# Kernel tuning notes

Hardware: AMD Instinct MI355X
Metric: run time of the kernel (lower is better)

Reference implementation:

```python
import jax, jax.numpy as jnp
import numpy as np
from jax import lax

B, D, H, E, TOPK = 4096, 512, 1024, 16, 4


def setup_inputs() -> dict:
    key = jax.random.key(0)
    ks = jax.random.split(key, 7)
    s = 0.02
    return {
        "x": jax.random.normal(ks[0], (B, D), jnp.float32),
        "gate_x": jax.random.normal(ks[1], (B, D), jnp.float32),
        "w_gate": jax.random.normal(ks[2], (D, E), jnp.float32) * s,
        "w1": jax.random.normal(ks[3], (E, D, H), jnp.float32) * s,
        "b1": jax.random.normal(ks[4], (E, H), jnp.float32) * s,
        "w2": jax.random.normal(ks[5], (E, H, D), jnp.float32) * s,
        "b2": jax.random.normal(ks[6], (E, D), jnp.float32) * s,
        "k": TOPK,
    }


def _cv_squared(v):
    # torch .var() is unbiased (ddof=1)
    eps = 1e-10
    return jnp.var(v, ddof=1) / (jnp.mean(v) ** 2 + eps)


def reference(x, gate_x, w_gate, w1, b1, w2, b2, k):
    # --- noisy_top_k_gating with train=False (clean logits path) ---
    logits = gate_x @ w_gate                      # [B, E]
    top_logits, top_idx = lax.top_k(logits, min(k + 1, E))
    topk_logits = top_logits[:, :k]               # [B, k]
    topk_idx = top_idx[:, :k]                     # [B, k]
    topk_gates = jax.nn.softmax(topk_logits, axis=1)
    batch_ar = jnp.arange(logits.shape[0])[:, None]
    gates = jnp.zeros_like(logits).at[batch_ar, topk_idx].set(topk_gates)  # [B, E]

    load = (gates > 0).sum(axis=0).astype(jnp.float32)   # [E]
    importance = gates.sum(axis=0)                        # [E]
    loss = _cv_squared(importance) + _cv_squared(load)

    # --- dispatch / per-expert MLP / weighted combine ---
    # Mathematically identical to SparseDispatcher: output[b] = sum_e gates[b,e]*MLP_e(x[b]).
    # Expressed as a vectorized per-expert GEMM; zero gates null out non-routed experts.
    h = jax.nn.relu(jnp.einsum('bd,edh->ebh', x, w1) + b1[:, None, :])  # [E, B, H]
    expert_out = jnp.einsum('ebh,eho->ebo', h, w2) + b2[:, None, :]      # [E, B, D]
    y = jnp.einsum('be,ebo->bo', gates, expert_out)                      # [B, D]
    return y, loss
```

## Files before the change

### kernel.cpp

```cpp
#include <hip/hip_runtime.h>
#include <cstdint>
#include <cstddef>

#define B_TOK 4096
#define DIM   512
#define HID   1024
#define NEXP  16
#define NSLOT 4

typedef __bf16 bf16x8 __attribute__((ext_vector_type(8)));
typedef float  f32x4  __attribute__((ext_vector_type(4)));
typedef unsigned short ushort8 __attribute__((ext_vector_type(8)));
typedef unsigned short ushort4v __attribute__((ext_vector_type(4)));

static __device__ __forceinline__ unsigned short f2bf(float f) {
    union { float f; unsigned u; } v; v.f = f;
    unsigned r = v.u + 0x7FFFu + ((v.u >> 16) & 1u);
    return (unsigned short)(r >> 16);
}
static __device__ __forceinline__ float bf2f(unsigned short u) {
    union { unsigned u; float f; } v; v.u = (unsigned)u << 16; return v.f;
}

static __device__ __forceinline__ void gl_lds16(const unsigned short* g, unsigned short* l) {
    __builtin_amdgcn_global_load_lds(
        (const __attribute__((address_space(1))) unsigned int*)(const void*)g,
        (__attribute__((address_space(3))) unsigned int*)(void*)l, 16, 0, 0);
}

static __device__ __forceinline__ bf16x8 fragRD(const unsigned short* s, int row, int ks) {
    int byte = row * 128 + ((ks * 2) ^ ((row & 7) << 4));
    return *(const bf16x8*)((const char*)s + byte);
}

#define LOGITS_OFF 0x0000000u
#define LTOK_OFF   0x0100000u
#define LGATE_OFF  0x0140000u
#define CTRL_OFF   0x0180000u
#define PMAP_OFF   0x01A0000u
#define XBF_OFF    0x0200000u
#define W1T_OFF    0x0600000u
#define W2T_OFF    0x1600000u
#define H_OFF      0x2600000u
#define YS_OFF     W1T_OFF

__global__ __launch_bounds__(256) void k_init(
        int* cnt, float* imp,
        const float* __restrict__ x, unsigned short* __restrict__ xbf,
        const float* __restrict__ w1, unsigned short* __restrict__ w1t,
        const float* __restrict__ gx, const float* __restrict__ wg,
        float* __restrict__ logits) {
    __shared__ unsigned short T[64][74];
    const int bid = blockIdx.x;
    const int t = threadIdx.x;
    if (bid < 1024) {
        int row = bid * 4 + (t >> 6);
        int l = t & 63;
        int e = l & 15;
        int c = l >> 4;
        const float* xr = gx + (size_t)row * DIM + c * 128;
        const float* wc = wg + (size_t)(c * 128) * NEXP + e;
        float s = 0.0f;
        #pragma unroll 8
        for (int d = 0; d < 128; d += 4) {
            float4 v = *(const float4*)(xr + d);
            s += v.x * wc[(d + 0) * NEXP] + v.y * wc[(d + 1) * NEXP]
               + v.z * wc[(d + 2) * NEXP] + v.w * wc[(d + 3) * NEXP];
        }
        s += __shfl_xor(s, 16);
        s += __shfl_xor(s, 32);
        if (l < NEXP) logits[row * NEXP + l] = s;
        return;
    }
    if (bid < 2048) {
        int i = (bid - 1024) * 256 + t;
        const float4* s = (const float4*)(x + (size_t)i * 8);
        float4 a = s[0], b = s[1];
        ushort8 v = { f2bf(a.x), f2bf(a.y), f2bf(a.z), f2bf(a.w),
                      f2bf(b.x), f2bf(b.y), f2bf(b.z), f2bf(b.w) };
        *(ushort8*)(xbf + (size_t)i * 8) = v;
        if (bid == 1024 && t < NEXP) { cnt[t] = 0; imp[t] = 0.0f; }
        return;
    }
    const int idx = bid - 2048;
    const int ktiles = DIM >> 6;
    const int e   = idx >> 7;
    const int rem = idx & 127;
    const int k0 = (rem % ktiles) * 64;
    const int n0 = (rem / ktiles) * 64;
    const int kr = t >> 4, n4 = (t & 15) * 4;
    #pragma unroll
    for (int it = 0; it < 4; it++) {
        int k = kr + it * 16;
        float4 v = *(const float4*)(w1 + ((size_t)e * DIM + k0 + k) * HID + n0 + n4);
        T[n4 + 0][k] = f2bf(v.x);
        T[n4 + 1][k] = f2bf(v.y);
        T[n4 + 2][k] = f2bf(v.z);
        T[n4 + 3][k] = f2bf(v.w);
    }
    __syncthreads();
    const int nn = t >> 3, k8 = (t & 7) * 8;
    #pragma unroll
    for (int rep = 0; rep < 2; rep++) {
        int n = nn + rep * 32;
        ushort8 o;
        #pragma unroll
        for (int i = 0; i < 8; i++) o[i] = T[n][k8 + i];
        *(ushort8*)(w1t + ((size_t)e * HID + n0 + n) * DIM + k0 + k8) = o;
    }
}

__global__ __launch_bounds__(64) void k_route(const float* __restrict__ logits,
                        int* __restrict__ cnt, float* __restrict__ imp,
                        int* __restrict__ ltok, float* __restrict__ lgate,
                        int* __restrict__ posmap) {
    __shared__ int   lcnt[NEXP];
    __shared__ float limp[NEXP];
    __shared__ int   lbase[NEXP];
    const int t = threadIdx.x;
    if (t < NEXP) { lcnt[t] = 0; limp[t] = 0.0f; }
    __syncthreads();

    const int b = blockIdx.x * 64 + t;
    const float4* lp = (const float4*)(logits + (size_t)b * NEXP);
    float4 q0 = lp[0], q1 = lp[1], q2 = lp[2], q3 = lp[3];
    float lg[NEXP] = { q0.x, q0.y, q0.z, q0.w, q1.x, q1.y, q1.z, q1.w,
                       q2.x, q2.y, q2.z, q2.w, q3.x, q3.y, q3.z, q3.w };

    int idx[NSLOT]; float val[NSLOT];
    unsigned used = 0;
    #pragma unroll
    for (int j = 0; j < NSLOT; j++) {
        float bv = -1e30f; int bi = 0;
        #pragma unroll
        for (int i = 0; i < NEXP; i++) {
            bool ok = !((used >> i) & 1u);
            if (ok && lg[i] > bv) { bv = lg[i]; bi = i; }
        }
        idx[j] = bi; val[j] = bv; used |= (1u << bi);
    }
    float m = val[0];
    float ex[NSLOT]; float sum = 0.0f;
    #pragma unroll
    for (int j = 0; j < NSLOT; j++) { ex[j] = __expf(val[j] - m); sum += ex[j]; }
    float inv = 1.0f / sum;

    int   lpos[NSLOT];
    float gv[NSLOT];
    #pragma unroll
    for (int j = 0; j < NSLOT; j++) {
        gv[j] = ex[j] * inv;
        lpos[j] = atomicAdd(&lcnt[idx[j]], 1);
        atomicAdd(&limp[idx[j]], gv[j]);
    }
    __syncthreads();
    if (t < NEXP) {
        lbase[t] = atomicAdd(&cnt[t], lcnt[t]);
        atomicAdd(&imp[t], limp[t]);
    }
    __syncthreads();
    #pragma unroll
    for (int j = 0; j < NSLOT; j++) {
        int e = idx[j];
        int p = lbase[e] + lpos[j];
        ltok[e * B_TOK + p]  = b;
        lgate[e * B_TOK + p] = gv[j];
        posmap[b * NSLOT + j] = (e << 12) | p;
    }
}

__global__ void k_prep(int* __restrict__ ctrl, float* __restrict__ out_loss) {
    const int* cnt = ctrl;
    const float* imp = (const float*)(ctrl + 16);
    int* bases = ctrl + 32;
    int* np    = ctrl + 48;
    int* pairs = ctrl + 64;
    int l = threadIdx.x;
    if (l >= 16) return;
    int base = 0, poff = 0;
    #pragma unroll
    for (int j = 0; j < 16; j++) {
        int cj = cnt[j];
        base += (j < l) ? cj : 0;
        poff += (j < l) ? ((cj + 127) >> 7) : 0;
    }
    bases[l] = base;
    int c = cnt[l];
    int ntile = (c + 127) >> 7;
    for (int i = 0; i < ntile; i++) pairs[poff + i] = (l << 16) | i;
    if (l == 15) *np = poff + ntile;

    float cf = (float)c, im = imp[l];
    float sc = cf, si = im;
    #pragma unroll
    for (int m = 8; m >= 1; m >>= 1) { sc += __shfl_xor(sc, m, 16); si += __shfl_xor(si, m, 16); }
    float ml = sc / 16.0f, mi = si / 16.0f;
    float dc = cf - ml, di = im - mi;
    float vc = dc * dc, vi = di * di;
    #pragma unroll
    for (int m = 8; m >= 1; m >>= 1) { vc += __shfl_xor(vc, m, 16); vi += __shfl_xor(vi, m, 16); }
    vc /= 15.0f; vi /= 15.0f;
    if (l == 0) *out_loss = vi / (mi * mi + 1e-10f) + vc / (ml * ml + 1e-10f);
}

__global__ __launch_bounds__(256, 3) void k_ffn1(
        const unsigned short* __restrict__ xbf, const unsigned short* __restrict__ w1t,
        const float* __restrict__ b1, const int* __restrict__ ctrl,
        const int* __restrict__ ltok, unsigned short* __restrict__ hbuf,
        const float* __restrict__ w2, unsigned short* __restrict__ w2t) {
    __shared__ __align__(16) unsigned short Sh[2][128 * 64];
    __shared__ int toks[128];

    const int orig = blockIdx.x;
    const int tid = threadIdx.x;

    if (orig >= 1280) {
        unsigned short (*T)[74] = (unsigned short (*)[74])&Sh[0][0];
        const int idx = orig - 1280;
        const int ktiles = HID >> 6;
        const int e   = idx >> 7;
        const int rem = idx & 127;
        const int k0 = (rem % ktiles) * 64;
        const int n0 = (rem / ktiles) * 64;
        const int kr = tid >> 4, n4 = (tid & 15) * 4;
        #pragma unroll
        for (int it = 0; it < 4; it++) {
            int k = kr + it * 16;
            float4 v = *(const float4*)(w2 + ((size_t)e * HID + k0 + k) * DIM + n0 + n4);
            T[n4 + 0][k] = f2bf(v.x);
            T[n4 + 1][k] = f2bf(v.y);
            T[n4 + 2][k] = f2bf(v.z);
            T[n4 + 3][k] = f2bf(v.w);
        }
        __syncthreads();
        const int nn = tid >> 3, k8 = (tid & 7) * 8;
        #pragma unroll
        for (int rep = 0; rep < 2; rep++) {
            int n = nn + rep * 32;
            ushort8 o;
            #pragma unroll
            for (int i = 0; i < 8; i++) o[i] = T[n][k8 + i];
            *(ushort8*)(w2t + ((size_t)e * DIM + n0 + n) * HID + k0 + k8) = o;
        }
        return;
    }

    const int wgid = (orig & 7) * 160 + (orig >> 3);
    const int pi = wgid >> 3, nt = wgid & 7;
    if (pi >= ctrl[48]) return;
    const int pr = ctrl[64 + pi];
    const int e  = pr >> 16;
    const int mt = pr & 0xffff;
    const int n_e = ctrl[e];
    const int base = ctrl[32 + e];
    const int row0 = mt * 128;

    unsigned short* As = &Sh[0][0];
    unsigned short* Bs = &Sh[1][0];

    const int lane = tid & 63, wv = tid >> 6;
    const int wm = wv >> 1, wn = wv & 1;
    const int lr = lane & 15, lq = lane >> 4;

    if (tid < 128) toks[tid] = ltok[e * B_TOK + min(row0 + tid, n_e - 1)];
    __syncthreads();

    const unsigned short* a_src[4];
    const unsigned short* b_src[4];
    #pragma unroll
    for (int c = 0; c < 4; c++) {
        int s = (wv * 4 + c) * 64 + lane;
        int r = s >> 3;
        int kc = (s & 7) ^ (r & 7);
        a_src[c] = xbf + (size_t)toks[r] * DIM + kc * 8;
        b_src[c] = w1t + ((size_t)(e * HID + nt * 128 + r)) * DIM + kc * 8;
    }

    f32x4 acc[4][4];
    #pragma unroll
    for (int m = 0; m < 4; m++)
        #pragma unroll
        for (int n = 0; n < 4; n++) acc[m][n] = (f32x4){0.f, 0.f, 0.f, 0.f};

    for (int kt = 0; kt < DIM; kt += 64) {
        #pragma unroll
        for (int c = 0; c < 4; c++) {
            gl_lds16(a_src[c] + kt, &As[(wv * 4 + c) * 512]);
            gl_lds16(b_src[c] + kt, &Bs[(wv * 4 + c) * 512]);
        }
        __syncthreads();
        #pragma unroll
        for (int kk = 0; kk < 64; kk += 32) {
            bf16x8 af[4], bfr[4];
            #pragma unroll
            for (int i = 0; i < 4; i++) {
                af[i]  = fragRD(As, wm * 64 + i * 16 + lr, kk + lq * 8);
                bfr[i] = fragRD(Bs, wn * 64 + i * 16 + lr, kk + lq * 8);
            }
            #pragma unroll
            for (int i = 0; i < 4; i++)
                #pragma unroll
                for (int j = 0; j < 4; j++)
                    acc[i][j] = __builtin_amdgcn_mfma_f32_16x16x32_bf16(af[i], bfr[j], acc[i][j], 0, 0, 0);
        }
        __syncthreads();
    }

    unsigned short* St = &Sh[0][0];
    #pragma unroll
    for (int j = 0; j < 4; j++) {
        int col = wn * 64 + j * 16 + lr;
        float bias = b1[e * HID + nt * 128 + col];
        #pragma unroll
        for (int i = 0; i < 4; i++) {
            #pragma unroll
            for (int q = 0; q < 4; q++) {
                int row = wm * 64 + i * 16 + lq * 4 + q;
                float v = acc[i][j][q] + bias;
                v = v > 0.0f ? v : 0.0f;
                int byte = row * 256 + ((col * 2) ^ ((row & 7) << 4));
                *(unsigned short*)((char*)St + byte) = f2bf(v);
            }
        }
    }
    __syncthreads();
    #pragma unroll
    for (int r8 = 0; r8 < 8; r8++) {
        int idx = r8 * 2048 + tid * 8;
        int row = idx >> 7;
        int colw = idx & 127;
        int pos = row0 + row;
        if (pos < n_e) {
            int byte = row * 256 + ((colw * 2) ^ ((row & 7) << 4));
            ushort8 o = *(const ushort8*)((const char*)St + byte);
            *(ushort8*)(hbuf + (size_t)(base + pos) * HID + nt * 128 + colw) = o;
        }
    }
}

__global__ __launch_bounds__(256, 3) void k_ffn2(
        const unsigned short* __restrict__ hbuf, const unsigned short* __restrict__ w2t,
        const float* __restrict__ b2, const int* __restrict__ ctrl,
        const int* __restrict__ ltok, const float* __restrict__ lgate,
        unsigned short* __restrict__ yslot) {
    const int orig = blockIdx.x;
    const int wgid = (orig & 7) * 72 + (orig >> 3);
    const int pi = wgid >> 2, nt = wgid & 3;
    if (pi >= ctrl[48]) return;
    const int pr = ctrl[64 + pi];
    const int e  = pr >> 16;
    const int mt = pr & 0xffff;
    const int n_e = ctrl[e];
    const int base = ctrl[32 + e];
    const int row0 = mt * 128;

    __shared__ __align__(16) unsigned short Sh[2][128 * 64];
    __shared__ float gts[128];
    unsigned short* As = &Sh[0][0];
    unsigned short* Bs = &Sh[1][0];

    const int tid = threadIdx.x;
    const int lane = tid & 63, wv = tid >> 6;
    const int wm = wv >> 1, wn = wv & 1;
    const int lr = lane & 15, lq = lane >> 4;

    if (tid < 128) {
        int p = min(row0 + tid, n_e - 1);
        gts[tid] = lgate[e * B_TOK + p];
    }
    __syncthreads();

    const unsigned short* a_src[4];
    const unsigned short* b_src[4];
    #pragma unroll
    for (int c = 0; c < 4; c++) {
        int s = (wv * 4 + c) * 64 + lane;
        int r = s >> 3;
        int kc = (s & 7) ^ (r & 7);
        a_src[c] = hbuf + (size_t)(base + min(row0 + r, n_e - 1)) * HID + kc * 8;
        b_src[c] = w2t + ((size_t)(e * DIM + nt * 128 + r)) * HID + kc * 8;
    }

    f32x4 acc[4][4];
    #pragma unroll
    for (int m = 0; m < 4; m++)
        #pragma unroll
        for (int n = 0; n < 4; n++) acc[m][n] = (f32x4){0.f, 0.f, 0.f, 0.f};

    for (int kt = 0; kt < HID; kt += 64) {
        #pragma unroll
        for (int c = 0; c < 4; c++) {
            gl_lds16(a_src[c] + kt, &As[(wv * 4 + c) * 512]);
            gl_lds16(b_src[c] + kt, &Bs[(wv * 4 + c) * 512]);
        }
        __syncthreads();
        #pragma unroll
        for (int kk = 0; kk < 64; kk += 32) {
            bf16x8 af[4], bfr[4];
            #pragma unroll
            for (int i = 0; i < 4; i++) {
                af[i]  = fragRD(As, wm * 64 + i * 16 + lr, kk + lq * 8);
                bfr[i] = fragRD(Bs, wn * 64 + i * 16 + lr, kk + lq * 8);
            }
            #pragma unroll
            for (int i = 0; i < 4; i++)
                #pragma unroll
                for (int j = 0; j < 4; j++)
                    acc[i][j] = __builtin_amdgcn_mfma_f32_16x16x32_bf16(af[i], bfr[j], acc[i][j], 0, 0, 0);
        }
        __syncthreads();
    }

    unsigned short* St = &Sh[0][0];
    #pragma unroll
    for (int j = 0; j < 4; j++) {
        int col = wn * 64 + j * 16 + lr;
        float bias = b2[e * DIM + nt * 128 + col];
        #pragma unroll
        for (int i = 0; i < 4; i++) {
            #pragma unroll
            for (int q = 0; q < 4; q++) {
                int row = wm * 64 + i * 16 + lq * 4 + q;
                float v = (acc[i][j][q] + bias) * gts[row];
                int byte = row * 256 + ((col * 2) ^ ((row & 7) << 4));
                *(unsigned short*)((char*)St + byte) = f2bf(v);
            }
        }
    }
    __syncthreads();
    #pragma unroll
    for (int r8 = 0; r8 < 8; r8++) {
        int idx = r8 * 2048 + tid * 8;
        int row = idx >> 7;
        int colw = idx & 127;
        int pos = row0 + row;
        if (pos < n_e) {
            int byte = row * 256 + ((colw * 2) ^ ((row & 7) << 4));
            ushort8 o = *(const ushort8*)((const char*)St + byte);
            *(ushort8*)(yslot + (size_t)(base + pos) * DIM + nt * 128 + colw) = o;
        }
    }
}

__global__ __launch_bounds__(256) void k_gather(
        const unsigned short* __restrict__ yslot, const int* __restrict__ posmap,
        const int* __restrict__ ctrl, float* __restrict__ y) {
    const int tok = blockIdx.x * 4 + (threadIdx.x >> 6);
    const int c8  = (threadIdx.x & 63) * 8;
    float s[8] = {0.f, 0.f, 0.f, 0.f, 0.f, 0.f, 0.f, 0.f};
    #pragma unroll
    for (int j = 0; j < NSLOT; j++) {
        int pm = posmap[tok * NSLOT + j];
        int e = pm >> 12, p = pm & 4095;
        size_t row = (size_t)(ctrl[32 + e] + p);
        ushort8 v = *(const ushort8*)(yslot + row * DIM + c8);
        #pragma unroll
        for (int q = 0; q < 8; q++) s[q] += bf2f(v[q]);
    }
    float4 o0 = {s[0], s[1], s[2], s[3]};
    float4 o1 = {s[4], s[5], s[6], s[7]};
    *(float4*)(y + (size_t)tok * DIM + c8)     = o0;
    *(float4*)(y + (size_t)tok * DIM + c8 + 4) = o1;
}

extern "C" void kernel_launch(void* const* d_in, const int* in_sizes, int n_in,
                              void* d_out, int out_size, void* d_ws, size_t ws_size,
                              hipStream_t stream) {
    const float* x  = (const float*)d_in[0];
    const float* gx = (const float*)d_in[1];
    const float* wg = (const float*)d_in[2];
    const float* w1 = (const float*)d_in[3];
    const float* b1 = (const float*)d_in[4];
    const float* w2 = (const float*)d_in[5];
    const float* b2 = (const float*)d_in[6];
    float* out = (float*)d_out;

    char* ws = (char*)d_ws;
    float* logits = (float*)(ws + LOGITS_OFF);
    int*   ltok   = (int*)(ws + LTOK_OFF);
    float* lgate  = (float*)(ws + LGATE_OFF);
    int*   ctrl   = (int*)(ws + CTRL_OFF);
    int*   cnt    = ctrl;
    float* imp    = (float*)(ctrl + 16);
    int*   posmap = (int*)(ws + PMAP_OFF);
    unsigned short* xbf   = (unsigned short*)(ws + XBF_OFF);
    unsigned short* w1t   = (unsigned short*)(ws + W1T_OFF);
    unsigned short* w2t   = (unsigned short*)(ws + W2T_OFF);
    unsigned short* hbuf  = (unsigned short*)(ws + H_OFF);
    unsigned short* yslot = (unsigned short*)(ws + YS_OFF);

    hipLaunchKernelGGL(k_init, dim3(4096), dim3(256), 0, stream,
                       cnt, imp, x, xbf, w1, w1t, gx, wg, logits);
    hipLaunchKernelGGL(k_route, dim3(B_TOK / 64), dim3(64), 0, stream,
                       logits, cnt, imp, ltok, lgate, posmap);
    hipLaunchKernelGGL(k_prep, dim3(1), dim3(64), 0, stream, ctrl,
                       out + (size_t)B_TOK * DIM);
    hipLaunchKernelGGL(k_ffn1, dim3(3328), dim3(256), 0, stream,
                       xbf, w1t, b1, ctrl, ltok, hbuf, w2, w2t);
    hipLaunchKernelGGL(k_ffn2, dim3(576), dim3(256), 0, stream,
                       hbuf, w2t, b2, ctrl, ltok, lgate, yslot);
    hipLaunchKernelGGL(k_gather, dim3(B_TOK / 4), dim3(256), 0, stream,
                       yslot, posmap, ctrl, out);
}
```

Before: 91.43 us.

## Enlarge FFN1 GEMM tiles to 256x256 with 512-thread blocks

Switches the first expert GEMM from 128x128 tiles with 256 threads to 256x256 tiles with 512 threads, using a separate 256-row tile list built in the prep kernel. Each wave now computes 128x64 outputs, which raises MFMA work per LDS fragment load and halves redundant global loads of x and w1. The w2 transpose blocks are repacked two per workgroup, and the epilogue is written in two halves to fit shared memory. The larger tiles cut the number of workgroups and waste more rows on partially filled expert tiles, while the bigger accumulator raises register pressure and may reduce occupancy.

```diff
diff --git a/kernel.cpp b/kernel.cpp
--- a/kernel.cpp
+++ b/kernel.cpp
@@ -173,22 +173,25 @@
     const int* cnt = ctrl;
     const float* imp = (const float*)(ctrl + 16);
     int* bases = ctrl + 32;
-    int* np    = ctrl + 48;
-    int* pairs = ctrl + 64;
+    int* pairs128 = ctrl + 64;
+    int* pairs256 = ctrl + 256;
     int l = threadIdx.x;
     if (l >= 16) return;
-    int base = 0, poff = 0;
+    int base = 0, poff = 0, poff256 = 0;
     #pragma unroll
     for (int j = 0; j < 16; j++) {
         int cj = cnt[j];
-        base += (j < l) ? cj : 0;
-        poff += (j < l) ? ((cj + 127) >> 7) : 0;
+        base    += (j < l) ? cj : 0;
+        poff    += (j < l) ? ((cj + 127) >> 7) : 0;
+        poff256 += (j < l) ? ((cj + 255) >> 8) : 0;
     }
     bases[l] = base;
     int c = cnt[l];
-    int ntile = (c + 127) >> 7;
-    for (int i = 0; i < ntile; i++) pairs[poff + i] = (l << 16) | i;
-    if (l == 15) *np = poff + ntile;
+    int nt128 = (c + 127) >> 7;
+    for (int i = 0; i < nt128; i++) pairs128[poff + i] = (l << 16) | i;
+    int nt256 = (c + 255) >> 8;
+    for (int i = 0; i < nt256; i++) pairs256[poff256 + i] = (l << 16) | i;
+    if (l == 15) { ctrl[48] = poff + nt128; ctrl[49] = poff256 + nt256; }
 
     float cf = (float)c, im = imp[l];
     float sc = cf, si = im;
@@ -203,26 +206,28 @@
     if (l == 0) *out_loss = vi / (mi * mi + 1e-10f) + vc / (ml * ml + 1e-10f);
 }
 
-__global__ __launch_bounds__(256, 3) void k_ffn1(
+__global__ __launch_bounds__(512, 2) void k_ffn1(
         const unsigned short* __restrict__ xbf, const unsigned short* __restrict__ w1t,
         const float* __restrict__ b1, const int* __restrict__ ctrl,
         const int* __restrict__ ltok, unsigned short* __restrict__ hbuf,
         const float* __restrict__ w2, unsigned short* __restrict__ w2t) {
-    __shared__ __align__(16) unsigned short Sh[2][128 * 64];
-    __shared__ int toks[128];
+    __shared__ __align__(16) unsigned short Sh[2][256 * 64];
+    __shared__ int toks[256];
 
     const int orig = blockIdx.x;
     const int tid = threadIdx.x;
 
-    if (orig >= 1280) {
-        unsigned short (*T)[74] = (unsigned short (*)[74])&Sh[0][0];
-        const int idx = orig - 1280;
+    if (orig >= 384) {
+        const int half = tid >> 8;
+        const int t    = tid & 255;
+        unsigned short (*T)[74] = (unsigned short (*)[74])(&Sh[0][0] + half * 4736);
+        const int idx = (orig - 384) * 2 + half;
         const int ktiles = HID >> 6;
         const int e   = idx >> 7;
         const int rem = idx & 127;
         const int k0 = (rem % ktiles) * 64;
         const int n0 = (rem / ktiles) * 64;
-        const int kr = tid >> 4, n4 = (tid & 15) * 4;
+        const int kr = t >> 4, n4 = (t & 15) * 4;
         #pragma unroll
         for (int it = 0; it < 4; it++) {
             int k = kr + it * 16;
@@ -233,7 +238,7 @@
             T[n4 + 3][k] = f2bf(v.w);
         }
         __syncthreads();
-        const int nn = tid >> 3, k8 = (tid & 7) * 8;
+        const int nn = t >> 3, k8 = (t & 7) * 8;
         #pragma unroll
         for (int rep = 0; rep < 2; rep++) {
             int n = nn + rep * 32;
@@ -245,40 +250,39 @@
         return;
     }
 
-    const int wgid = (orig & 7) * 160 + (orig >> 3);
-    const int pi = wgid >> 3, nt = wgid & 7;
-    if (pi >= ctrl[48]) return;
-    const int pr = ctrl[64 + pi];
+    const int pi = orig >> 2, nt = orig & 3;
+    if (pi >= ctrl[49]) return;
+    const int pr = ctrl[256 + pi];
     const int e  = pr >> 16;
     const int mt = pr & 0xffff;
     const int n_e = ctrl[e];
     const int base = ctrl[32 + e];
-    const int row0 = mt * 128;
+    const int row0 = mt * 256;
 
     unsigned short* As = &Sh[0][0];
     unsigned short* Bs = &Sh[1][0];
 
     const int lane = tid & 63, wv = tid >> 6;
-    const int wm = wv >> 1, wn = wv & 1;
+    const int wm = wv >> 2, wn = wv & 3;
     const int lr = lane & 15, lq = lane >> 4;
 
-    if (tid < 128) toks[tid] = ltok[e * B_TOK + min(row0 + tid, n_e - 1)];
+    if (tid < 256) toks[tid] = ltok[e * B_TOK + min(row0 + tid, n_e - 1)];
     __syncthreads();
 
     const unsigned short* a_src[4];
     const unsigned short* b_src[4];
     #pragma unroll
     for (int c = 0; c < 4; c++) {
-        int s = (wv * 4 + c) * 64 + lane;
-        int r = s >> 3;
-        int kc = (s & 7) ^ (r & 7);
+        int cid = (wv * 4 + c) * 64 + lane;
+        int r = cid >> 3;
+        int kc = (cid & 7) ^ (r & 7);
         a_src[c] = xbf + (size_t)toks[r] * DIM + kc * 8;
-        b_src[c] = w1t + ((size_t)(e * HID + nt * 128 + r)) * DIM + kc * 8;
-    }
-
-    f32x4 acc[4][4];
-    #pragma unroll
-    for (int m = 0; m < 4; m++)
+        b_src[c] = w1t + ((size_t)(e * HID + nt * 256 + r)) * DIM + kc * 8;
+    }
+
+    f32x4 acc[8][4];
+    #pragma unroll
+    for (int m = 0; m < 8; m++)
         #pragma unroll
         for (int n = 0; n < 4; n++) acc[m][n] = (f32x4){0.f, 0.f, 0.f, 0.f};
 
@@ -291,14 +295,13 @@
         __syncthreads();
         #pragma unroll
         for (int kk = 0; kk < 64; kk += 32) {
-            bf16x8 af[4], bfr[4];
-            #pragma unroll
-            for (int i = 0; i < 4; i++) {
-                af[i]  = fragRD(As, wm * 64 + i * 16 + lr, kk + lq * 8);
-                bfr[i] = fragRD(Bs, wn * 64 + i * 16 + lr, kk + lq * 8);
-            }
-            #pragma unroll
-            for (int i = 0; i < 4; i++)
+            bf16x8 af[8], bfr[4];
+            #pragma unroll
+            for (int i = 0; i < 8; i++) af[i] = fragRD(As, wm * 128 + i * 16 + lr, kk + lq * 8);
+            #pragma unroll
+            for (int j = 0; j < 4; j++) bfr[j] = fragRD(Bs, wn * 64 + j * 16 + lr, kk + lq * 8);
+            #pragma unroll
+            for (int i = 0; i < 8; i++)
                 #pragma unroll
                 for (int j = 0; j < 4; j++)
                     acc[i][j] = __builtin_amdgcn_mfma_f32_16x16x32_bf16(af[i], bfr[j], acc[i][j], 0, 0, 0);
@@ -308,40 +311,46 @@
 
     unsigned short* St = &Sh[0][0];
     #pragma unroll
-    for (int j = 0; j < 4; j++) {
-        int col = wn * 64 + j * 16 + lr;
-        float bias = b1[e * HID + nt * 128 + col];
-        #pragma unroll
-        for (int i = 0; i < 4; i++) {
-            #pragma unroll
-            for (int q = 0; q < 4; q++) {
-                int row = wm * 64 + i * 16 + lq * 4 + q;
-                float v = acc[i][j][q] + bias;
-                v = v > 0.0f ? v : 0.0f;
-                int byte = row * 256 + ((col * 2) ^ ((row & 7) << 4));
-                *(unsigned short*)((char*)St + byte) = f2bf(v);
+    for (int h = 0; h < 2; h++) {
+        if (wm == h) {
+            #pragma unroll
+            for (int j = 0; j < 4; j++) {
+                int col = wn * 64 + j * 16 + lr;
+                float bias = b1[e * HID + nt * 256 + col];
+                #pragma unroll
+                for (int i = 0; i < 8; i++) {
+                    #pragma unroll
+                    for (int q = 0; q < 4; q++) {
+                        int row = i * 16 + lq * 4 + q;
+                        float v = acc[i][j][q] + bias;
+                        v = v > 0.0f ? v : 0.0f;
+                        int byte = row * 512 + ((col * 2) ^ ((row & 7) << 4));
+                        *(unsigned short*)((char*)St + byte) = f2bf(v);
+                    }
+                }
             }
         }
-    }
-    __syncthreads();
-    #pragma unroll
-    for (int r8 = 0; r8 < 8; r8++) {
-        int idx = r8 * 2048 + tid * 8;
-        int row = idx >> 7;
-        int colw = idx & 127;
-        int pos = row0 + row;
-        if (pos < n_e) {
-            int byte = row * 256 + ((colw * 2) ^ ((row & 7) << 4));
-            ushort8 o = *(const ushort8*)((const char*)St + byte);
-            *(ushort8*)(hbuf + (size_t)(base + pos) * HID + nt * 128 + colw) = o;
-        }
+        __syncthreads();
+        #pragma unroll
+        for (int r8 = 0; r8 < 8; r8++) {
+            int idx = r8 * 4096 + tid * 8;
+            int row = idx >> 8;
+            int colw = idx & 255;
+            int pos = row0 + h * 128 + row;
+            if (pos < n_e) {
+                int byte = row * 512 + ((colw * 2) ^ ((row & 7) << 4));
+                ushort8 o = *(const ushort8*)((const char*)St + byte);
+                *(ushort8*)(hbuf + (size_t)(base + pos) * HID + nt * 256 + colw) = o;
+            }
+        }
+        __syncthreads();
     }
 }
 
 __global__ __launch_bounds__(256, 3) void k_ffn2(
         const unsigned short* __restrict__ hbuf, const unsigned short* __restrict__ w2t,
         const float* __restrict__ b2, const int* __restrict__ ctrl,
-        const int* __restrict__ ltok, const float* __restrict__ lgate,
+        const float* __restrict__ lgate,
         unsigned short* __restrict__ yslot) {
     const int orig = blockIdx.x;
     const int wgid = (orig & 7) * 72 + (orig >> 3);
@@ -495,10 +504,10 @@
                        logits, cnt, imp, ltok, lgate, posmap);
     hipLaunchKernelGGL(k_prep, dim3(1), dim3(64), 0, stream, ctrl,
                        out + (size_t)B_TOK * DIM);
-    hipLaunchKernelGGL(k_ffn1, dim3(3328), dim3(256), 0, stream,
+    hipLaunchKernelGGL(k_ffn1, dim3(1408), dim3(512), 0, stream,
                        xbf, w1t, b1, ctrl, ltok, hbuf, w2, w2t);
     hipLaunchKernelGGL(k_ffn2, dim3(576), dim3(256), 0, stream,
-                       hbuf, w2t, b2, ctrl, ltok, lgate, yslot);
+                       hbuf, w2t, b2, ctrl, lgate, yslot);
     hipLaunchKernelGGL(k_gather, dim3(B_TOK / 4), dim3(256), 0, stream,
                        yslot, posmap, ctrl, out);
 }
```

Measured after the change: 112.6 us. +23.2%, slower.
